# Performance work log

Hardware: AMD Instinct MI355X
Metric: run time of the kernel (lower is better)

The kernel has to match this reference:

```python
import jax, jax.numpy as jnp
import numpy as np

N_NODES = 50000
N_EDGES = 800000
HIDDEN = 64
OUT = 16
N_LAYERS = 3


def setup_inputs() -> dict:
    key = jax.random.key(0)
    ks = jax.random.split(key, 8)
    s = 1.0 / np.sqrt(HIDDEN)
    x = jax.random.normal(ks[0], (N_NODES, HIDDEN), dtype=jnp.float32)
    edge_index = jax.random.randint(ks[1], (2, N_EDGES), 0, N_NODES, dtype=jnp.int64)
    # SAGEConv params per layer: lin_l (neighbor path, with bias), lin_r (root path, no bias)
    Wl = jax.random.uniform(ks[2], (N_LAYERS, HIDDEN, HIDDEN), jnp.float32, -s, s)
    bl = jax.random.uniform(ks[3], (N_LAYERS, HIDDEN), jnp.float32, -s, s)
    Wr = jax.random.uniform(ks[4], (N_LAYERS, HIDDEN, HIDDEN), jnp.float32, -s, s)
    W_out = jax.random.uniform(ks[5], (HIDDEN, OUT), jnp.float32, -s, s)
    b_out = jax.random.uniform(ks[6], (OUT,), jnp.float32, -s, s)
    return {"x": x, "edge_index": edge_index, "Wl": Wl, "bl": bl, "Wr": Wr,
            "W_out": W_out, "b_out": b_out}


def reference(x, edge_index, Wl, bl, Wr, W_out, b_out):
    n = x.shape[0]
    src, dst = edge_index[0], edge_index[1]
    # in-degree for mean aggregation (clamped to 1 to avoid div-by-zero)
    deg = jax.ops.segment_sum(jnp.ones((src.shape[0],), x.dtype), dst, num_segments=n)
    deg = jnp.maximum(deg, 1.0)[:, None]  # [N, 1]
    for l in range(N_LAYERS):
        msg = x[src]                                            # [E, H] gather
        agg = jax.ops.segment_sum(msg, dst, num_segments=n) / deg  # scatter-mean [N, H]
        # SAGEConv: lin_l(agg) + lin_r(x)  (lin_r has no bias)
        x = agg @ Wl[l] + bl[l] + x @ Wr[l]
        x = jax.nn.relu(x)
    return x @ W_out + b_out
```

## Files before the change

### kernel.cpp

```cpp
#include <hip/hip_runtime.h>
#include <hip/hip_bf16.h>

#define NN 50000
#define NE 800000
#define HD 64
#define OD 16
#define CAP 64
#define TILES 3125
#define AST 72
#define NPART 8
#define PSZ 6250

typedef unsigned short u16;
typedef unsigned int u32;
typedef __attribute__((ext_vector_type(8))) short short8;
typedef __attribute__((ext_vector_type(4))) float f32x4;

__device__ __forceinline__ float bf2f(u16 v) { return __uint_as_float(((u32)v) << 16); }
__device__ __forceinline__ u16 f2bf(float f) {
  __hip_bfloat16 h = __float2bfloat16(f);
  return *reinterpret_cast<u16*>(&h);
}
__device__ __forceinline__ float ldf(const void* p, long i, bool f32m) {
  return f32m ? ((const float*)p)[i] : bf2f(((const u16*)p)[i]);
}
__device__ __forceinline__ int edge_at(const void* eidx, long pos, bool i64) {
  return i64 ? (int)((const long long*)eidx)[pos] : ((const int*)eidx)[pos];
}

__global__ void k_detect(const u32* __restrict__ e32, const u16* __restrict__ xu,
                         int* flags) {
  int i = blockIdx.x * blockDim.x + threadIdx.x;
  if (i < 4096) {
    if (e32[2 * i + 1] != 0u) atomicOr(&flags[0], 1);
  }
  if (i < 65536) {
    u16 v = xu[i];
    int e = (v >> 7) & 0xFF;
    if (v != 0 && (e < 100 || e > 140)) atomicAdd(&flags[1], 1);
  }
}

__global__ __launch_bounds__(256) void k_prep(
    const void* __restrict__ x,
    const void* __restrict__ Wl, const void* __restrict__ bl,
    const void* __restrict__ Wr, const void* __restrict__ Wo,
    const void* __restrict__ bo,
    u16* __restrict__ xA, u16* __restrict__ wfrag, u16* __restrict__ pfrag,
    float* __restrict__ blf, float* __restrict__ bof,
    const int* __restrict__ flags) {
  bool f32m = flags[1] > 1000;
  int i = blockIdx.x * blockDim.x + threadIdx.x;
  if (f32m) {
    float4 v = ((const float4*)x)[i];
    u32 lo = (u32)f2bf(v.x) | ((u32)f2bf(v.y) << 16);
    u32 hi = (u32)f2bf(v.z) | ((u32)f2bf(v.w) << 16);
    ((u32*)xA)[2 * i] = lo;
    ((u32*)xA)[2 * i + 1] = hi;
  }
  if (i < 3 * 16 * 64 * 8) {
    int j = i & 7, lane = (i >> 3) & 63, f = (i >> 9) & 15, l = i >> 13;
    int s = f >> 2, c = f & 3;
    int k = 32 * s + ((lane >> 4) << 3) + j;
    int n = (c << 4) + (lane & 15);
    long wbase = (long)l * HD * HD;
    float v = (k < HD) ? ldf(Wl, wbase + (long)k * HD + n, f32m)
                       : ldf(Wr, wbase + (long)(k - HD) * HD + n, f32m);
    wfrag[i] = f2bf(v);
  }
  if (i < 2 * 64 * 8) {
    int j = i & 7, lane = (i >> 3) & 63, s = i >> 9;
    int k = 32 * s + ((lane >> 4) << 3) + j;
    pfrag[i] = f2bf(ldf(Wo, (long)k * OD + (lane & 15), f32m));
  }
  if (i < 3 * HD) blf[i] = ldf(bl, i, f32m);
  if (i < OD) bof[i] = ldf(bo, i, f32m);
}

__global__ __launch_bounds__(256) void k_scat3(
    const void* __restrict__ eidx,
    int* __restrict__ deg, u16* __restrict__ csr, u32* __restrict__ spill,
    int* __restrict__ flags) {
  bool i64 = (flags[0] == 0);
  int g = blockIdx.x & 7;
  int lo = g * PSZ, hi = lo + PSZ;
  int base = (blockIdx.x >> 3) * 256 + threadIdx.x;
  for (int e = base; e < NE; e += 65536) {
    int dst = edge_at(eidx, (long)NE + e, i64);
    if (dst >= lo && dst < hi) {
      int src = edge_at(eidx, e, i64);
      int pos = atomicAdd(&deg[dst], 1);
      if (pos < CAP) csr[(long)dst * CAP + pos] = (u16)src;
      else {
        int sp = atomicAdd(&flags[4], 1);
        spill[sp] = (u32)dst * 50000u + (u32)src;
      }
    }
  }
}

__global__ __launch_bounds__(256, 8) void k_fused(
    const u16* __restrict__ xin_bf, const u16* __restrict__ xin_f32m,
    u16* __restrict__ xout,
    const int* __restrict__ deg, const u16* __restrict__ csr,
    const u32* __restrict__ spill,
    const u16* __restrict__ wfrag, const u16* __restrict__ pfrag,
    const float* __restrict__ bl3, const float* __restrict__ bof,
    void* __restrict__ outp, int layer, int doProj,
    const int* __restrict__ flags) {
  __shared__ __align__(16) u16 aw[16 * AST];
  __shared__ float sbl[HD];
  __shared__ float sbo[OD];
  if (threadIdx.x < HD) sbl[threadIdx.x] = bl3[layer * HD + threadIdx.x];
  if (threadIdx.x < OD) sbo[threadIdx.x] = bof[threadIdx.x];
  bool f32m = flags[1] > 1000;
  int spillcnt = __builtin_amdgcn_readfirstlane(flags[4]);
  const u16* xin = f32m ? xin_f32m : xin_bf;
  const u32* x32 = (const u32*)xin;

  int lane = threadIdx.x & 63;
  int w = threadIdx.x >> 6;
  int nb = blockIdx.x * 16;
  int fl = lane & 31;
  int half = lane >> 5;
  u32* aw32 = (u32*)aw;

  for (int g = 0; g < 4; ++g) {
    int n = nb + 4 * w + g;
    int dtot = __builtin_amdgcn_readfirstlane(deg[n]);
    int d = dtot < CAP ? dtot : CAP;
    const u16* cr = csr + (long)n * CAP;
    int idx = (lane < d) ? (int)cr[lane] : 0;
    float ax0 = 0.f, ay0 = 0.f, ax1 = 0.f, ay1 = 0.f;
    for (int j = 0; j < d; j += 8) {
#pragma unroll
      for (int p = 0; p < 4; ++p) {
        int se = __builtin_amdgcn_readlane(idx, j + 2 * p);
        int so = __builtin_amdgcn_readlane(idx, j + 2 * p + 1);
        int s = half ? so : se;
        u32 v = x32[(long)s * 32 + fl];
        int m = j + 2 * p + half;
        v = (m < d) ? v : 0u;
        float vlo = __uint_as_float(v << 16);
        float vhi = __uint_as_float(v & 0xffff0000u);
        if (p & 1) { ax1 += vlo; ay1 += vhi; }
        else       { ax0 += vlo; ay0 += vhi; }
      }
    }
    float ax = ax0 + ax1, ay = ay0 + ay1;
    ax += __shfl_xor(ax, 32);
    ay += __shfl_xor(ay, 32);
    if (spillcnt > 0) {
      for (int base = 0; base < spillcnt; base += 64) {
        u32 p = (base + lane < spillcnt) ? spill[base + lane] : 0xffffffffu;
        u32 dd = p / 50000u;
        u32 ss = p - dd * 50000u;
        unsigned long long mk = __ballot(dd == (u32)n);
        while (mk) {
          int j = __builtin_ctzll(mk);
          mk &= mk - 1;
          int s = __builtin_amdgcn_readlane((int)ss, j);
          u32 v = x32[(long)s * 32 + fl];
          ax += __uint_as_float(v << 16);
          ay += __uint_as_float(v & 0xffff0000u);
        }
      }
    }
    float rd = 1.0f / (float)(dtot > 0 ? dtot : 1);
    if (half == 0)
      aw32[(4 * w + g) * (AST / 2) + fl] =
          (u32)f2bf(ax * rd) | ((u32)f2bf(ay * rd) << 16);
  }
  __syncthreads();

  int quad = lane >> 4, m16 = lane & 15;
  short8 a0 = *(const short8*)(aw + m16 * AST + quad * 8);
  short8 a1 = *(const short8*)(aw + m16 * AST + 32 + quad * 8);
  const u16* xrow = xin + (long)(nb + m16) * HD;
  short8 x2 = *(const short8*)(xrow + quad * 8);
  short8 x3 = *(const short8*)(xrow + 32 + quad * 8);
  int c = w;
  const short8* bp = (const short8*)(wfrag + (long)layer * 16 * 64 * 8);
  short8 b0 = bp[(0 * 4 + c) * 64 + lane];
  short8 b1 = bp[(1 * 4 + c) * 64 + lane];
  short8 b2 = bp[(2 * 4 + c) * 64 + lane];
  short8 b3 = bp[(3 * 4 + c) * 64 + lane];
  float bb = sbl[c * 16 + m16];
  f32x4 acc = (f32x4){bb, bb, bb, bb};
  acc = __builtin_amdgcn_mfma_f32_16x16x32_bf16(a0, b0, acc, 0, 0, 0);
  acc = __builtin_amdgcn_mfma_f32_16x16x32_bf16(a1, b1, acc, 0, 0, 0);
  acc = __builtin_amdgcn_mfma_f32_16x16x32_bf16(x2, b2, acc, 0, 0, 0);
  acc = __builtin_amdgcn_mfma_f32_16x16x32_bf16(x3, b3, acc, 0, 0, 0);
  __syncthreads();

#pragma unroll
  for (int r = 0; r < 4; ++r)
    aw[(quad * 4 + r) * AST + c * 16 + m16] = f2bf(fmaxf(acc[r], 0.f));
  __syncthreads();

  if (!doProj) {
    int row = threadIdx.x >> 4, ch = threadIdx.x & 15;
    uint2 v = *(const uint2*)(aw + row * AST + ch * 4);
    *(uint2*)(xout + (long)(nb + row) * HD + ch * 4) = v;
  } else if (w == 0) {
    short8 pa0 = *(const short8*)(aw + m16 * AST + quad * 8);
    short8 pa1 = *(const short8*)(aw + m16 * AST + 32 + quad * 8);
    const short8* pb = (const short8*)pfrag;
    short8 pb0 = pb[lane];
    short8 pb1 = pb[64 + lane];
    float bv = sbo[m16];
    f32x4 pacc = (f32x4){bv, bv, bv, bv};
    pacc = __builtin_amdgcn_mfma_f32_16x16x32_bf16(pa0, pb0, pacc, 0, 0, 0);
    pacc = __builtin_amdgcn_mfma_f32_16x16x32_bf16(pa1, pb1, pacc, 0, 0, 0);
    if (f32m) {
      float* o = (float*)outp;
#pragma unroll
      for (int r = 0; r < 4; ++r)
        o[(long)(nb + quad * 4 + r) * OD + m16] = pacc[r];
    } else {
      u16* o = (u16*)outp;
#pragma unroll
      for (int r = 0; r < 4; ++r)
        o[(long)(nb + quad * 4 + r) * OD + m16] = f2bf(pacc[r]);
    }
  }
}

extern "C" void kernel_launch(void* const* d_in, const int* in_sizes, int n_in,
                              void* d_out, int out_size, void* d_ws, size_t ws_size,
                              hipStream_t stream) {
  const void* x = d_in[0];
  const void* eidx = d_in[1];
  const void* Wl = d_in[2];
  const void* bl = d_in[3];
  const void* Wr = d_in[4];
  const void* Wo = d_in[5];
  const void* bo = d_in[6];

  char* w = (char*)d_ws;
  size_t off = 0;
  int* flags = (int*)(w + off);     off += 256;
  int* deg = (int*)(w + off);       off += (size_t)NN * 4 + 192;
  size_t memset_bytes = off;
  u16* csr = (u16*)(w + off);       off += (size_t)NN * CAP * 2;
  u32* spill = (u32*)(w + off);     off += (size_t)NE * 4;
  u16* wfrag = (u16*)(w + off);     off += 3 * 16 * 64 * 8 * 2;
  u16* pfrag = (u16*)(w + off);     off += 2 * 64 * 8 * 2;
  float* blf = (float*)(w + off);   off += 3 * HD * 4;
  float* bof = (float*)(w + off);   off += 256;
  u16* xA = (u16*)(w + off);        off += (size_t)NN * HD * 2;
  u16* xB = (u16*)(w + off);        off += (size_t)NN * HD * 2;

  hipMemsetAsync(flags, 0, memset_bytes, stream);

  k_detect<<<256, 256, 0, stream>>>((const u32*)eidx, (const u16*)x, flags);
  k_prep<<<3125, 256, 0, stream>>>(x, Wl, bl, Wr, Wo, bo,
                                   xA, wfrag, pfrag, blf, bof, flags);
  k_scat3<<<2048, 256, 0, stream>>>(eidx, deg, csr, spill, flags);

  k_fused<<<TILES, 256, 0, stream>>>((const u16*)x, xA, xB, deg, csr, spill,
                                     wfrag, pfrag, blf, bof, (void*)0, 0, 0, flags);
  k_fused<<<TILES, 256, 0, stream>>>(xB, xB, xA, deg, csr, spill,
                                     wfrag, pfrag, blf, bof, (void*)0, 1, 0, flags);
  k_fused<<<TILES, 256, 0, stream>>>(xA, xA, (u16*)0, deg, csr, spill,
                                     wfrag, pfrag, blf, bof, d_out, 2, 1, flags);
}
```

Measured before the change: 207.6 us.

## Merge detect, prep and scatter kernels; prefetch CSR indices and deepen gather ILP

Folds the separate detection, weight-prep and edge-scatter kernels into one launch. Each wave now runs the dtype and index-width detection itself with a ballot over a small sample, so the global flag round-trip goes away. In the fused layer kernel, the four node degrees are loaded as one int4 and all CSR index rows are prefetched up front. The gather loop now issues 16 neighbor loads before accumulating, to raise memory-level parallelism. The cost is redundant per-wave detection reads, a smaller detection sample that could misclassify the input, and higher register use.

```diff
diff --git a/kernel.cpp b/kernel.cpp
--- a/kernel.cpp
+++ b/kernel.cpp
@@ -8,7 +8,7 @@
 #define CAP 64
 #define TILES 3125
 #define AST 72
-#define NPART 8
+#define SCATB 2048
 #define PSZ 6250
 
 typedef unsigned short u16;
@@ -28,80 +28,76 @@
   return i64 ? (int)((const long long*)eidx)[pos] : ((const int*)eidx)[pos];
 }
 
-__global__ void k_detect(const u32* __restrict__ e32, const u16* __restrict__ xu,
-                         int* flags) {
-  int i = blockIdx.x * blockDim.x + threadIdx.x;
-  if (i < 4096) {
-    if (e32[2 * i + 1] != 0u) atomicOr(&flags[0], 1);
-  }
-  if (i < 65536) {
-    u16 v = xu[i];
-    int e = (v >> 7) & 0xFF;
-    if (v != 0 && (e < 100 || e > 140)) atomicAdd(&flags[1], 1);
-  }
-}
-
-__global__ __launch_bounds__(256) void k_prep(
-    const void* __restrict__ x,
+__device__ __forceinline__ bool detect_i64(const u32* e32, int lane) {
+  return __ballot(e32[2 * lane + 1] != 0u) == 0ull;
+}
+__device__ __forceinline__ bool detect_f32(const u32* x32, int lane) {
+  u32 v = x32[lane] & 0xffffu;
+  int e = (int)((v >> 7) & 0xff);
+  bool wild = (v != 0u) && (e < 100 || e > 140);
+  return __popcll(__ballot(wild)) > 16;
+}
+
+__global__ __launch_bounds__(256) void k_pre(
+    const void* __restrict__ x, const void* __restrict__ eidx,
     const void* __restrict__ Wl, const void* __restrict__ bl,
     const void* __restrict__ Wr, const void* __restrict__ Wo,
     const void* __restrict__ bo,
+    int* __restrict__ deg, u16* __restrict__ csr, u32* __restrict__ spill,
     u16* __restrict__ xA, u16* __restrict__ wfrag, u16* __restrict__ pfrag,
     float* __restrict__ blf, float* __restrict__ bof,
-    const int* __restrict__ flags) {
-  bool f32m = flags[1] > 1000;
-  int i = blockIdx.x * blockDim.x + threadIdx.x;
-  if (f32m) {
-    float4 v = ((const float4*)x)[i];
-    u32 lo = (u32)f2bf(v.x) | ((u32)f2bf(v.y) << 16);
-    u32 hi = (u32)f2bf(v.z) | ((u32)f2bf(v.w) << 16);
-    ((u32*)xA)[2 * i] = lo;
-    ((u32*)xA)[2 * i + 1] = hi;
-  }
-  if (i < 3 * 16 * 64 * 8) {
-    int j = i & 7, lane = (i >> 3) & 63, f = (i >> 9) & 15, l = i >> 13;
-    int s = f >> 2, c = f & 3;
-    int k = 32 * s + ((lane >> 4) << 3) + j;
-    int n = (c << 4) + (lane & 15);
-    long wbase = (long)l * HD * HD;
-    float v = (k < HD) ? ldf(Wl, wbase + (long)k * HD + n, f32m)
-                       : ldf(Wr, wbase + (long)(k - HD) * HD + n, f32m);
-    wfrag[i] = f2bf(v);
-  }
-  if (i < 2 * 64 * 8) {
-    int j = i & 7, lane = (i >> 3) & 63, s = i >> 9;
-    int k = 32 * s + ((lane >> 4) << 3) + j;
-    pfrag[i] = f2bf(ldf(Wo, (long)k * OD + (lane & 15), f32m));
-  }
-  if (i < 3 * HD) blf[i] = ldf(bl, i, f32m);
-  if (i < OD) bof[i] = ldf(bo, i, f32m);
-}
-
-__global__ __launch_bounds__(256) void k_scat3(
-    const void* __restrict__ eidx,
-    int* __restrict__ deg, u16* __restrict__ csr, u32* __restrict__ spill,
     int* __restrict__ flags) {
-  bool i64 = (flags[0] == 0);
-  int g = blockIdx.x & 7;
-  int lo = g * PSZ, hi = lo + PSZ;
-  int base = (blockIdx.x >> 3) * 256 + threadIdx.x;
-  for (int e = base; e < NE; e += 65536) {
-    int dst = edge_at(eidx, (long)NE + e, i64);
-    if (dst >= lo && dst < hi) {
-      int src = edge_at(eidx, e, i64);
-      int pos = atomicAdd(&deg[dst], 1);
-      if (pos < CAP) csr[(long)dst * CAP + pos] = (u16)src;
-      else {
-        int sp = atomicAdd(&flags[4], 1);
-        spill[sp] = (u32)dst * 50000u + (u32)src;
-      }
-    }
+  int lane = threadIdx.x & 63;
+  if (blockIdx.x < SCATB) {
+    bool i64 = detect_i64((const u32*)eidx, lane);
+    int g = blockIdx.x & 7;
+    int lo = g * PSZ, hi = lo + PSZ;
+    int base = (blockIdx.x >> 3) * 256 + threadIdx.x;
+    for (int e = base; e < NE; e += 65536) {
+      int dst = edge_at(eidx, (long)NE + e, i64);
+      if (dst >= lo && dst < hi) {
+        int src = edge_at(eidx, e, i64);
+        int pos = atomicAdd(&deg[dst], 1);
+        if (pos < CAP) csr[(long)dst * CAP + pos] = (u16)src;
+        else {
+          int sp = atomicAdd(&flags[4], 1);
+          spill[sp] = (u32)dst * 50000u + (u32)src;
+        }
+      }
+    }
+  } else {
+    bool f32m = detect_f32((const u32*)x, lane);
+    int i = (blockIdx.x - SCATB) * 256 + threadIdx.x;
+    if (f32m) {
+      float4 v = ((const float4*)x)[i];
+      u32 lo = (u32)f2bf(v.x) | ((u32)f2bf(v.y) << 16);
+      u32 hi = (u32)f2bf(v.z) | ((u32)f2bf(v.w) << 16);
+      ((u32*)xA)[2 * i] = lo;
+      ((u32*)xA)[2 * i + 1] = hi;
+    }
+    if (i < 3 * 16 * 64 * 8) {
+      int j = i & 7, ln = (i >> 3) & 63, f = (i >> 9) & 15, l = i >> 13;
+      int s = f >> 2, c = f & 3;
+      int k = 32 * s + ((ln >> 4) << 3) + j;
+      int n = (c << 4) + (ln & 15);
+      long wbase = (long)l * HD * HD;
+      float v = (k < HD) ? ldf(Wl, wbase + (long)k * HD + n, f32m)
+                         : ldf(Wr, wbase + (long)(k - HD) * HD + n, f32m);
+      wfrag[i] = f2bf(v);
+    }
+    if (i < 2 * 64 * 8) {
+      int j = i & 7, ln = (i >> 3) & 63, s = i >> 9;
+      int k = 32 * s + ((ln >> 4) << 3) + j;
+      pfrag[i] = f2bf(ldf(Wo, (long)k * OD + (ln & 15), f32m));
+    }
+    if (i < 3 * HD) blf[i] = ldf(bl, i, f32m);
+    if (i < OD) bof[i] = ldf(bo, i, f32m);
   }
 }
 
 __global__ __launch_bounds__(256, 8) void k_fused(
     const u16* __restrict__ xin_bf, const u16* __restrict__ xin_f32m,
-    u16* __restrict__ xout,
+    const u32* __restrict__ xorig32, u16* __restrict__ xout,
     const int* __restrict__ deg, const u16* __restrict__ csr,
     const u32* __restrict__ spill,
     const u16* __restrict__ wfrag, const u16* __restrict__ pfrag,
@@ -113,36 +109,50 @@
   __shared__ float sbo[OD];
   if (threadIdx.x < HD) sbl[threadIdx.x] = bl3[layer * HD + threadIdx.x];
   if (threadIdx.x < OD) sbo[threadIdx.x] = bof[threadIdx.x];
-  bool f32m = flags[1] > 1000;
+  int lane = threadIdx.x & 63;
+  bool f32m = detect_f32(xorig32, lane);
   int spillcnt = __builtin_amdgcn_readfirstlane(flags[4]);
   const u16* xin = f32m ? xin_f32m : xin_bf;
   const u32* x32 = (const u32*)xin;
 
-  int lane = threadIdx.x & 63;
   int w = threadIdx.x >> 6;
   int nb = blockIdx.x * 16;
   int fl = lane & 31;
   int half = lane >> 5;
   u32* aw32 = (u32*)aw;
-
+  int n0 = nb + 4 * w;
+
+  int4 dv = *(const int4*)(deg + n0);
+  int dt[4] = {__builtin_amdgcn_readfirstlane(dv.x),
+               __builtin_amdgcn_readfirstlane(dv.y),
+               __builtin_amdgcn_readfirstlane(dv.z),
+               __builtin_amdgcn_readfirstlane(dv.w)};
+  int idx[4];
+#pragma unroll
   for (int g = 0; g < 4; ++g) {
-    int n = nb + 4 * w + g;
-    int dtot = __builtin_amdgcn_readfirstlane(deg[n]);
+    int d = dt[g] < CAP ? dt[g] : CAP;
+    idx[g] = (lane < d) ? (int)csr[(long)(n0 + g) * CAP + lane] : 0;
+  }
+
+  for (int g = 0; g < 4; ++g) {
+    int dtot = dt[g];
     int d = dtot < CAP ? dtot : CAP;
-    const u16* cr = csr + (long)n * CAP;
-    int idx = (lane < d) ? (int)cr[lane] : 0;
     float ax0 = 0.f, ay0 = 0.f, ax1 = 0.f, ay1 = 0.f;
-    for (int j = 0; j < d; j += 8) {
-#pragma unroll
-      for (int p = 0; p < 4; ++p) {
-        int se = __builtin_amdgcn_readlane(idx, j + 2 * p);
-        int so = __builtin_amdgcn_readlane(idx, j + 2 * p + 1);
+    for (int j = 0; j < d; j += 16) {
+      u32 v[8];
+#pragma unroll
+      for (int p = 0; p < 8; ++p) {
+        int se = __builtin_amdgcn_readlane(idx[g], j + 2 * p);
+        int so = __builtin_amdgcn_readlane(idx[g], j + 2 * p + 1);
         int s = half ? so : se;
-        u32 v = x32[(long)s * 32 + fl];
+        v[p] = x32[(long)s * 32 + fl];
+      }
+#pragma unroll
+      for (int p = 0; p < 8; ++p) {
         int m = j + 2 * p + half;
-        v = (m < d) ? v : 0u;
-        float vlo = __uint_as_float(v << 16);
-        float vhi = __uint_as_float(v & 0xffff0000u);
+        u32 vv = (m < d) ? v[p] : 0u;
+        float vlo = __uint_as_float(vv << 16);
+        float vhi = __uint_as_float(vv & 0xffff0000u);
         if (p & 1) { ax1 += vlo; ay1 += vhi; }
         else       { ax0 += vlo; ay0 += vhi; }
       }
@@ -151,6 +161,7 @@
     ax += __shfl_xor(ax, 32);
     ay += __shfl_xor(ay, 32);
     if (spillcnt > 0) {
+      int n = n0 + g;
       for (int base = 0; base < spillcnt; base += 64) {
         u32 p = (base + lane < spillcnt) ? spill[base + lane] : 0xffffffffu;
         u32 dd = p / 50000u;
@@ -253,15 +264,15 @@
 
   hipMemsetAsync(flags, 0, memset_bytes, stream);
 
-  k_detect<<<256, 256, 0, stream>>>((const u32*)eidx, (const u16*)x, flags);
-  k_prep<<<3125, 256, 0, stream>>>(x, Wl, bl, Wr, Wo, bo,
-                                   xA, wfrag, pfrag, blf, bof, flags);
-  k_scat3<<<2048, 256, 0, stream>>>(eidx, deg, csr, spill, flags);
-
-  k_fused<<<TILES, 256, 0, stream>>>((const u16*)x, xA, xB, deg, csr, spill,
+  k_pre<<<SCATB + 3125, 256, 0, stream>>>(x, eidx, Wl, bl, Wr, Wo, bo,
+                                          deg, csr, spill, xA, wfrag, pfrag,
+                                          blf, bof, flags);
+
+  const u32* xo32 = (const u32*)x;
+  k_fused<<<TILES, 256, 0, stream>>>((const u16*)x, xA, xo32, xB, deg, csr, spill,
                                      wfrag, pfrag, blf, bof, (void*)0, 0, 0, flags);
-  k_fused<<<TILES, 256, 0, stream>>>(xB, xB, xA, deg, csr, spill,
+  k_fused<<<TILES, 256, 0, stream>>>(xB, xB, xo32, xA, deg, csr, spill,
                                      wfrag, pfrag, blf, bof, (void*)0, 1, 0, flags);
-  k_fused<<<TILES, 256, 0, stream>>>(xA, xA, (u16*)0, deg, csr, spill,
+  k_fused<<<TILES, 256, 0, stream>>>(xA, xA, xo32, (u16*)0, deg, csr, spill,
                                      wfrag, pfrag, blf, bof, d_out, 2, 1, flags);
 }
```

After: 187.2 us. 1.11x faster.
